# Performance work log

Hardware: AMD Instinct MI355X
Metric: run time of the kernel (lower is better)

The kernel has to match this reference:

```python
import jax, jax.numpy as jnp
import numpy as np

N = 50000      # nodes
E = 1600000    # directed edges (avg degree 32)
IN_DIM = 64
OUT_DIM = 64


def setup_inputs() -> dict:
    key = jax.random.key(0)
    ks = jax.random.split(key, 8)
    mu = jax.random.normal(ks[0], (N, IN_DIM), dtype=jnp.float32)
    x = jax.random.normal(ks[1], (N, 1), dtype=jnp.float32)
    edge_index = jax.random.randint(ks[2], (2, E), 0, N, dtype=jnp.int64)
    edge_w = jax.random.uniform(ks[3], (E,), dtype=jnp.float32)
    # torch nn.Linear(in, out, bias=False) weight has shape [out, in]
    W1 = jax.random.normal(ks[4], (OUT_DIM, 1), dtype=jnp.float32) * (1.0 / 1.0)
    W2 = jax.random.normal(ks[5], (OUT_DIM, 1), dtype=jnp.float32) * (1.0 / 1.0)
    W3 = jax.random.normal(ks[6], (OUT_DIM, IN_DIM), dtype=jnp.float32) * (1.0 / np.sqrt(IN_DIM))
    W4 = jax.random.normal(ks[7], (OUT_DIM, 3 * OUT_DIM), dtype=jnp.float32) * (1.0 / np.sqrt(3 * OUT_DIM))
    return {"mu": mu, "x": x, "edge_index": edge_index, "edge_w": edge_w,
            "W1": W1, "W2": W2, "W3": W3, "W4": W4}


def reference(mu, x, edge_index, edge_w, W1, W2, W3, W4):
    relu = jax.nn.relu
    n_nodes = mu.shape[0]
    # per-node / per-edge embeddings
    h_x = relu(x @ W1.T)                       # [N, out]
    h_e = relu(edge_w[:, None] @ W2.T)         # [E, out]
    h_mu = relu(mu @ W3.T)                     # [N, out]
    dst = edge_index[1]                        # gather side (reverse-direction message passing)
    src = edge_index[0]                        # scatter side
    # gather, concat along feature dim -> [E, 3*out]
    cat_feat = jnp.concatenate([h_x[dst], h_e, h_mu[dst]], axis=1)
    # scatter_add over destination row 0 -> [N, 3*out]
    agg = jax.ops.segment_sum(cat_feat, src, num_segments=n_nodes)
    agg = relu(agg @ W4.T)                     # [N, out]
    return relu(h_x + h_mu + agg)
```

## Files before the change

### kernel.cpp

```cpp
#include <hip/hip_runtime.h>


#define KBINS 512
#define BCHUNK 4096
#define CAPB 4096
#define CAPL 3500
#define MAXW 98

typedef __attribute__((ext_vector_type(8))) short short8;
typedef __attribute__((ext_vector_type(4))) float f32x4;
typedef __attribute__((ext_vector_type(4))) unsigned short u16x4;

__device__ inline unsigned short to_bf16(float f) {
    unsigned u = __float_as_uint(f);
    return (unsigned short)((u + 0x7FFFu + ((u >> 16) & 1u)) >> 16);
}

__global__ void k_prep(const float* __restrict__ W1, const float* __restrict__ W2,
                       const float* __restrict__ W3, const float* __restrict__ W4,
                       short* __restrict__ gB1, short* __restrict__ gB2,
                       float* __restrict__ gvec, unsigned* __restrict__ gcursor) {
    __shared__ float sa[64], sb[64];
    int t = threadIdx.x;
    gcursor[t] = 0u;
    gcursor[256 + t] = 0u;
    if (t < 64) {
        float w1 = W1[t];
        sa[t] = fmaxf(w1, 0.f);
        sb[t] = fmaxf(-w1, 0.f);
        gvec[t] = sa[t];
        gvec[64 + t] = sb[t];
    }
    __syncthreads();
    if (t < 64) {
        float s1 = 0.f, s2 = 0.f, s3 = 0.f;
#pragma unroll 8
        for (int o = 0; o < 64; ++o) {
            float w4a = W4[t * 192 + o];
            float w4b = W4[t * 192 + 64 + o];
            s1 += w4a * sa[o];
            s2 += w4a * sb[o];
            s3 += w4b * fmaxf(W2[o], 0.f);
        }
        gvec[128 + t] = s1;
        gvec[192 + t] = s2;
        gvec[256 + t] = s3;
    }
    for (int idx = t; idx < 4096; idx += 256) {
        int j = idx >> 6, k = idx & 63;
        int lane = ((k >> 3) & 3) * 16 + (j & 15);
        int pos = (((j >> 4) * 2 + (k >> 5)) * 64 + lane) * 8 + (k & 7);
        gB1[pos] = (short)to_bf16(W3[idx]);
        gB2[pos] = (short)to_bf16(W4[j * 192 + 128 + k]);
    }
}

__global__ void __launch_bounds__(512, 8) k_hb(
    const float* __restrict__ mu, const float* __restrict__ x,
    const short* __restrict__ gB1, const short* __restrict__ gB2,
    const float* __restrict__ gvec,
    unsigned short* __restrict__ base, unsigned short* __restrict__ hc2,
    const int* __restrict__ ei, const float* __restrict__ ew,
    unsigned* __restrict__ gcursor, unsigned* __restrict__ bins,
    int N, int E) {
    __shared__ __align__(16) char smem[35840];
    short* sB1 = (short*)smem;
    short* sB2 = (short*)(smem + 8192);
    float* sAv = (float*)(smem + 16384);
    float* sBv = (float*)(smem + 16640);
    float* sVA = (float*)(smem + 16896);
    float* sVB = (float*)(smem + 17152);
    short* sA  = (short*)(smem + 17408);
    unsigned* cnt   = (unsigned*)smem;
    unsigned* basel = (unsigned*)(smem + 2048);
    unsigned* gbase = (unsigned*)(smem + 4096);
    unsigned* wsum  = (unsigned*)(smem + 6144);
    unsigned* wpre  = (unsigned*)(smem + 6176);
    unsigned* stage = (unsigned*)(smem + 6208);
    unsigned short* binof = (unsigned short*)(smem + 22592);

    int t = threadIdx.x;
    int wave = t >> 6, l = t & 63;

    for (int i = t; i < 512; i += 512) {
        ((short8*)sB1)[i] = ((const short8*)gB1)[i];
        ((short8*)sB2)[i] = ((const short8*)gB2)[i];
    }
    if (t >= 512 - 256) {
        int v = t - (512 - 256);
        if (v < 64) sAv[v] = gvec[v];
        else if (v < 128) sBv[v - 64] = gvec[64 + (v - 64)];
        else if (v < 192) sVA[v - 128] = gvec[128 + (v - 128)];
        else sVB[v - 192] = gvec[192 + (v - 192)];
    }
    __syncthreads();

    int n0 = (blockIdx.x * 8 + wave) * 16;
    if (n0 < N) {
        short* A1 = sA + wave * 2304 / 2;
        {
            int srow = l >> 2, scol = (l & 3) * 16;
            bool rok = (n0 + srow) < N;
            const float4* gp = (const float4*)(mu + (size_t)(n0 + srow) * 64 + scol);
            float4 m0 = {}, m1 = {}, m2 = {}, m3 = {};
            if (rok) { m0 = gp[0]; m1 = gp[1]; m2 = gp[2]; m3 = gp[3]; }
            short8 v0, v1;
            v0[0]=to_bf16(m0.x); v0[1]=to_bf16(m0.y); v0[2]=to_bf16(m0.z); v0[3]=to_bf16(m0.w);
            v0[4]=to_bf16(m1.x); v0[5]=to_bf16(m1.y); v0[6]=to_bf16(m1.z); v0[7]=to_bf16(m1.w);
            v1[0]=to_bf16(m2.x); v1[1]=to_bf16(m2.y); v1[2]=to_bf16(m2.z); v1[3]=to_bf16(m2.w);
            v1[4]=to_bf16(m3.x); v1[5]=to_bf16(m3.y); v1[6]=to_bf16(m3.z); v1[7]=to_bf16(m3.w);
            *(short8*)&A1[srow * 72 + scol] = v0;
            *(short8*)&A1[srow * 72 + scol + 8] = v1;
        }
        float pr[4], qr[4];
#pragma unroll
        for (int r = 0; r < 4; ++r) {
            int nr = n0 + (l >> 4) * 4 + r;
            float xv = (nr < N) ? x[nr] : 0.f;
            pr[r] = fmaxf(xv, 0.f);
            qr[r] = fmaxf(-xv, 0.f);
        }
        f32x4 acc[4] = {};
        {
            short8 a0 = *(const short8*)&A1[(l & 15) * 72 + ((l >> 4) * 8)];
            short8 a1 = *(const short8*)&A1[(l & 15) * 72 + 32 + ((l >> 4) * 8)];
#pragma unroll
            for (int jt = 0; jt < 4; ++jt) {
                short8 b0 = *(const short8*)&sB1[((jt * 2 + 0) * 64 + l) * 8];
                short8 b1 = *(const short8*)&sB1[((jt * 2 + 1) * 64 + l) * 8];
                acc[jt] = __builtin_amdgcn_mfma_f32_16x16x32_bf16(a0, b0, acc[jt], 0, 0, 0);
                acc[jt] = __builtin_amdgcn_mfma_f32_16x16x32_bf16(a1, b1, acc[jt], 0, 0, 0);
            }
        }
#pragma unroll
        for (int jt = 0; jt < 4; ++jt) {
            int jc = jt * 16 + (l & 15);
            float aj = sAv[jc], bj = sBv[jc];
#pragma unroll
            for (int r = 0; r < 4; ++r) {
                int row = (l >> 4) * 4 + r;
                float h = fmaxf(acc[jt][r], 0.f);
                A1[row * 72 + jc] = (short)to_bf16(h);
                int nr = n0 + row;
                if (nr < N) base[(size_t)nr * 64 + jc] = to_bf16(pr[r] * aj + qr[r] * bj + h);
            }
        }
        f32x4 acc2[4] = {};
        {
            short8 a0 = *(const short8*)&A1[(l & 15) * 72 + ((l >> 4) * 8)];
            short8 a1 = *(const short8*)&A1[(l & 15) * 72 + 32 + ((l >> 4) * 8)];
#pragma unroll
            for (int jt = 0; jt < 4; ++jt) {
                short8 b0 = *(const short8*)&sB2[((jt * 2 + 0) * 64 + l) * 8];
                short8 b1 = *(const short8*)&sB2[((jt * 2 + 1) * 64 + l) * 8];
                acc2[jt] = __builtin_amdgcn_mfma_f32_16x16x32_bf16(a0, b0, acc2[jt], 0, 0, 0);
                acc2[jt] = __builtin_amdgcn_mfma_f32_16x16x32_bf16(a1, b1, acc2[jt], 0, 0, 0);
            }
        }
#pragma unroll
        for (int jt = 0; jt < 4; ++jt) {
            int jc = jt * 16 + (l & 15);
            float vaj = sVA[jc], vbj = sVB[jc];
#pragma unroll
            for (int r = 0; r < 4; ++r) {
                int nr = n0 + (l >> 4) * 4 + r;
                if (nr < N)
                    hc2[(size_t)nr * 64 + jc] =
                        to_bf16(acc2[jt][r] + pr[r] * vaj + qr[r] * vbj);
            }
        }
    }
    __syncthreads();

    for (int c0 = blockIdx.x * BCHUNK; c0 < E; c0 += gridDim.x * BCHUNK) {
        cnt[t] = 0;
        __syncthreads();
        int mybin[8]; unsigned myrank[8]; unsigned myrec[8]; bool ok[8];
#pragma unroll
        for (int k = 0; k < 8; ++k) {
            int e = c0 + t + k * 512;
            ok[k] = (e < E);
            if (ok[k]) {
                int s = ei[e];
                int d = ei[E + e];
                unsigned wq = (unsigned)(ew[e] * 512.0f + 0.5f);
                if (wq > 511u) wq = 511u;
                unsigned b = ((unsigned)s * (unsigned)KBINS) / (unsigned)N;
                unsigned start = ((unsigned)b * (unsigned)N + KBINS - 1) / KBINS;
                unsigned sl = (unsigned)s - start;
                myrec[k] = (unsigned)d | (sl << 16) | (wq << 23);
                mybin[k] = (int)b;
                myrank[k] = atomicAdd(&cnt[b], 1u);
            }
        }
        __syncthreads();
        {
            unsigned v = cnt[t];
            unsigned sc = v;
#pragma unroll
            for (int off = 1; off < 64; off <<= 1) {
                unsigned u = (unsigned)__shfl_up((int)sc, off, 64);
                if (l >= off) sc += u;
            }
            if (l == 63) wsum[wave] = sc;
            __syncthreads();
            if (t < 8) {
                unsigned s = 0;
                for (int i = 0; i < t; ++i) s += wsum[i];
                wpre[t] = s;
            }
            __syncthreads();
            unsigned excl = sc - v + wpre[wave];
            basel[t] = excl;
            if (v) gbase[t] = atomicAdd(&gcursor[t], v);
        }
        __syncthreads();
#pragma unroll
        for (int k = 0; k < 8; ++k) if (ok[k]) {
            unsigned pos = basel[mybin[k]] + myrank[k];
            stage[pos] = myrec[k];
            binof[pos] = (unsigned short)mybin[k];
        }
        __syncthreads();
        int total = E - c0; if (total > BCHUNK) total = BCHUNK;
#pragma unroll
        for (int k = 0; k < 8; ++k) {
            int i = t + k * 512;
            if (i < total) {
                int b = binof[i];
                unsigned dst = gbase[b] + (unsigned)i - basel[b];
                if (dst < CAPB) bins[(size_t)b * CAPB + dst] = stage[i];
            }
        }
        __syncthreads();
    }
}

__global__ void __launch_bounds__(1024) k_agg(
    const unsigned short* __restrict__ hc2, const unsigned short* __restrict__ base,
    const unsigned* __restrict__ gcursor, const unsigned* __restrict__ bins,
    const float* __restrict__ gvec, float* __restrict__ out, int N) {
    __shared__ unsigned srec[CAPL];
    __shared__ unsigned hist[128];
    __shared__ unsigned sbase[128];
    __shared__ __align__(16) float svs[64];
    int b = blockIdx.x;
    int t = threadIdx.x;
    if (t < 128) hist[t] = 0;
    if (t >= 128 && t < 192) svs[t - 128] = gvec[256 + (t - 128)];
    int start = (b * N + KBINS - 1) / KBINS;
    int endn  = ((b + 1) * N + KBINS - 1) / KBINS;
    if (endn > N) endn = N;
    int W = endn - start;
    if (W > MAXW) W = MAXW;
    __syncthreads();
    int cntb = (int)gcursor[b];
    if (cntb > CAPB) cntb = CAPB;
    const unsigned* rec = bins + (size_t)b * CAPB;
    unsigned r[4]; unsigned rank[4]; bool ok[4];
#pragma unroll
    for (int k = 0; k < 4; ++k) {
        int i = t + k * 1024;
        ok[k] = (i < cntb);
        if (ok[k]) {
            r[k] = rec[i];
            rank[k] = atomicAdd(&hist[(r[k] >> 16) & 0x7Fu], 1u);
        }
    }
    __syncthreads();
    if (t < 64) {
        unsigned h0 = hist[2 * t], h1 = hist[2 * t + 1];
        unsigned s = h0 + h1;
#pragma unroll
        for (int off = 1; off < 64; off <<= 1) {
            unsigned u = (unsigned)__shfl_up((int)s, off, 64);
            if (t >= off) s += u;
        }
        sbase[2 * t]     = s - h1 - h0;
        sbase[2 * t + 1] = s - h1;
    }
    __syncthreads();
#pragma unroll
    for (int k = 0; k < 4; ++k) if (ok[k]) {
        unsigned pos = sbase[(r[k] >> 16) & 0x7Fu] + rank[k];
        if (pos < CAPL) srec[pos] = r[k];
    }
    __syncthreads();
    int wave = t >> 6, l = t & 63;
    int g = l >> 4, m = l & 15;
    f32x4 vsv = *(const f32x4*)&svs[m * 4];
    const float sc512 = 1.0f / 512.0f;
    for (int sl = wave; sl < W; sl += 16) {
        int beg = (int)sbase[sl];
        int end = beg + (int)hist[sl];
        if (beg > CAPL) beg = CAPL;
        if (end > CAPL) end = CAPL;
        f32x4 acc = {0.f, 0.f, 0.f, 0.f};
        float swn = 0.f;
        int i = beg;
        for (; i + 8 <= end; i += 8) {
            unsigned r0 = srec[i + g];
            unsigned r1 = srec[i + 4 + g];
            u16x4 u0 = *(const u16x4*)(hc2 + (size_t)(r0 & 0xFFFFu) * 64 + m * 4);
            u16x4 u1 = *(const u16x4*)(hc2 + (size_t)(r1 & 0xFFFFu) * 64 + m * 4);
            acc[0] += __uint_as_float((unsigned)u0[0] << 16);
            acc[1] += __uint_as_float((unsigned)u0[1] << 16);
            acc[2] += __uint_as_float((unsigned)u0[2] << 16);
            acc[3] += __uint_as_float((unsigned)u0[3] << 16);
            acc[0] += __uint_as_float((unsigned)u1[0] << 16);
            acc[1] += __uint_as_float((unsigned)u1[1] << 16);
            acc[2] += __uint_as_float((unsigned)u1[2] << 16);
            acc[3] += __uint_as_float((unsigned)u1[3] << 16);
            swn += (float)(r0 >> 23) + (float)(r1 >> 23);
        }
        for (; i < end; i += 4) {
            if (i + g < end) {
                unsigned r0 = srec[i + g];
                u16x4 u0 = *(const u16x4*)(hc2 + (size_t)(r0 & 0xFFFFu) * 64 + m * 4);
                acc[0] += __uint_as_float((unsigned)u0[0] << 16);
                acc[1] += __uint_as_float((unsigned)u0[1] << 16);
                acc[2] += __uint_as_float((unsigned)u0[2] << 16);
                acc[3] += __uint_as_float((unsigned)u0[3] << 16);
                swn += (float)(r0 >> 23);
            }
        }
#pragma unroll
        for (int off = 16; off < 64; off <<= 1) {
            acc[0] += __shfl_xor(acc[0], off, 64);
            acc[1] += __shfl_xor(acc[1], off, 64);
            acc[2] += __shfl_xor(acc[2], off, 64);
            acc[3] += __shfl_xor(acc[3], off, 64);
            swn    += __shfl_xor(swn, off, 64);
        }
        if (g == 0) {
            size_t gi = (size_t)(start + sl) * 64 + m * 4;
            u16x4 bv = *(const u16x4*)(base + gi);
            f32x4 o;
#pragma unroll
            for (int k = 0; k < 4; ++k) {
                float aggv = fmaxf(swn * (vsv[k] * sc512) + acc[k], 0.f);
                float bval = __uint_as_float(((unsigned)bv[k]) << 16);
                o[k] = fmaxf(bval + aggv, 0.f);
            }
            *(f32x4*)&out[gi] = o;
        }
    }
}

extern "C" void kernel_launch(void* const* d_in, const int* in_sizes, int n_in,
                              void* d_out, int out_size, void* d_ws, size_t ws_size,
                              hipStream_t stream) {
    const float* mu = (const float*)d_in[0];
    const float* x  = (const float*)d_in[1];
    const int*   ei = (const int*)d_in[2];
    const float* ew = (const float*)d_in[3];
    const float* W1 = (const float*)d_in[4];
    const float* W2 = (const float*)d_in[5];
    const float* W3 = (const float*)d_in[6];
    const float* W4 = (const float*)d_in[7];
    float* out = (float*)d_out;

    const int N = in_sizes[1];
    const int E = in_sizes[3];

    unsigned short* base = (unsigned short*)d_ws;
    unsigned short* hc2 = base + (size_t)N * 64;
    unsigned* bins = (unsigned*)(hc2 + (size_t)N * 64);
    unsigned* gcursor = bins + (size_t)KBINS * CAPB;
    short* gB1 = (short*)(gcursor + KBINS);
    short* gB2 = gB1 + 4096;
    float* gvec = (float*)(gB2 + 4096);

    k_prep<<<1, 256, 0, stream>>>(W1, W2, W3, W4, gB1, gB2, gvec, gcursor);

    int hblocks = (N + 127) / 128;
    int chunks = (E + BCHUNK - 1) / BCHUNK;
    int grid = hblocks > chunks ? hblocks : chunks;
    k_hb<<<grid, 512, 0, stream>>>(mu, x, gB1, gB2, gvec, base, hc2,
                                   ei, ew, gcursor, bins, N, E);

    k_agg<<<KBINS, 1024, 0, stream>>>(hc2, base, gcursor, bins, gvec, out, N);
}
```

Measured before the change: 59.76 us.

## Split bf16 node table into two 32-column planes for narrower gathers

The per-node bf16 feature table hc2 is now stored as two planes of 32 columns each instead of one 64-column row. The aggregation kernel makes two passes, one per plane, and each lane gathers 16 bytes (8 bf16) with 16 edges in flight per wave rather than 4. The goal is a smaller per-pass gather working set that fits cache better, plus more memory-level parallelism per load instruction. In exchange, the edge records and segment bounds are read twice, the wave reduction now spans more shuffle steps, and the loop body holds more accumulators.

```diff
diff --git a/kernel.cpp b/kernel.cpp
--- a/kernel.cpp
+++ b/kernel.cpp
@@ -81,6 +81,7 @@
 
     int t = threadIdx.x;
     int wave = t >> 6, l = t & 63;
+    size_t PN = (size_t)N * 32;
 
     for (int i = t; i < 512; i += 512) {
         ((short8*)sB1)[i] = ((const short8*)gB1)[i];
@@ -161,11 +162,13 @@
         for (int jt = 0; jt < 4; ++jt) {
             int jc = jt * 16 + (l & 15);
             float vaj = sVA[jc], vbj = sVB[jc];
+            size_t pb = (size_t)(jt >> 1) * PN;
+            int col = (jt & 1) * 16 + (l & 15);
 #pragma unroll
             for (int r = 0; r < 4; ++r) {
                 int nr = n0 + (l >> 4) * 4 + r;
                 if (nr < N)
-                    hc2[(size_t)nr * 64 + jc] =
+                    hc2[pb + (size_t)nr * 32 + col] =
                         to_bf16(acc2[jt][r] + pr[r] * vaj + qr[r] * vbj);
             }
         }
@@ -287,62 +290,66 @@
     }
     __syncthreads();
     int wave = t >> 6, l = t & 63;
-    int g = l >> 4, m = l & 15;
-    f32x4 vsv = *(const f32x4*)&svs[m * 4];
+    int g = l >> 2, m = l & 3;
+    size_t PN = (size_t)N * 32;
     const float sc512 = 1.0f / 512.0f;
-    for (int sl = wave; sl < W; sl += 16) {
-        int beg = (int)sbase[sl];
-        int end = beg + (int)hist[sl];
-        if (beg > CAPL) beg = CAPL;
-        if (end > CAPL) end = CAPL;
-        f32x4 acc = {0.f, 0.f, 0.f, 0.f};
-        float swn = 0.f;
-        int i = beg;
-        for (; i + 8 <= end; i += 8) {
-            unsigned r0 = srec[i + g];
-            unsigned r1 = srec[i + 4 + g];
-            u16x4 u0 = *(const u16x4*)(hc2 + (size_t)(r0 & 0xFFFFu) * 64 + m * 4);
-            u16x4 u1 = *(const u16x4*)(hc2 + (size_t)(r1 & 0xFFFFu) * 64 + m * 4);
-            acc[0] += __uint_as_float((unsigned)u0[0] << 16);
-            acc[1] += __uint_as_float((unsigned)u0[1] << 16);
-            acc[2] += __uint_as_float((unsigned)u0[2] << 16);
-            acc[3] += __uint_as_float((unsigned)u0[3] << 16);
-            acc[0] += __uint_as_float((unsigned)u1[0] << 16);
-            acc[1] += __uint_as_float((unsigned)u1[1] << 16);
-            acc[2] += __uint_as_float((unsigned)u1[2] << 16);
-            acc[3] += __uint_as_float((unsigned)u1[3] << 16);
-            swn += (float)(r0 >> 23) + (float)(r1 >> 23);
-        }
-        for (; i < end; i += 4) {
-            if (i + g < end) {
+#pragma unroll
+    for (int p = 0; p < 2; ++p) {
+        const unsigned short* hp = hc2 + (size_t)p * PN;
+        int fb = p * 32 + m * 8;
+        f32x4 vs0 = *(const f32x4*)&svs[fb];
+        f32x4 vs1 = *(const f32x4*)&svs[fb + 4];
+        for (int sl = wave; sl < W; sl += 16) {
+            int beg = (int)sbase[sl];
+            int end = beg + (int)hist[sl];
+            if (beg > CAPL) beg = CAPL;
+            if (end > CAPL) end = CAPL;
+            float acc[8] = {0.f, 0.f, 0.f, 0.f, 0.f, 0.f, 0.f, 0.f};
+            float swn = 0.f;
+            int i = beg;
+            for (; i + 32 <= end; i += 32) {
                 unsigned r0 = srec[i + g];
-                u16x4 u0 = *(const u16x4*)(hc2 + (size_t)(r0 & 0xFFFFu) * 64 + m * 4);
-                acc[0] += __uint_as_float((unsigned)u0[0] << 16);
-                acc[1] += __uint_as_float((unsigned)u0[1] << 16);
-                acc[2] += __uint_as_float((unsigned)u0[2] << 16);
-                acc[3] += __uint_as_float((unsigned)u0[3] << 16);
-                swn += (float)(r0 >> 23);
-            }
-        }
-#pragma unroll
-        for (int off = 16; off < 64; off <<= 1) {
-            acc[0] += __shfl_xor(acc[0], off, 64);
-            acc[1] += __shfl_xor(acc[1], off, 64);
-            acc[2] += __shfl_xor(acc[2], off, 64);
-            acc[3] += __shfl_xor(acc[3], off, 64);
-            swn    += __shfl_xor(swn, off, 64);
-        }
-        if (g == 0) {
-            size_t gi = (size_t)(start + sl) * 64 + m * 4;
-            u16x4 bv = *(const u16x4*)(base + gi);
-            f32x4 o;
-#pragma unroll
-            for (int k = 0; k < 4; ++k) {
-                float aggv = fmaxf(swn * (vsv[k] * sc512) + acc[k], 0.f);
-                float bval = __uint_as_float(((unsigned)bv[k]) << 16);
-                o[k] = fmaxf(bval + aggv, 0.f);
-            }
-            *(f32x4*)&out[gi] = o;
+                unsigned r1 = srec[i + 16 + g];
+                short8 u0 = *(const short8*)(hp + (size_t)(r0 & 0xFFFFu) * 32 + m * 8);
+                short8 u1 = *(const short8*)(hp + (size_t)(r1 & 0xFFFFu) * 32 + m * 8);
+#pragma unroll
+                for (int k = 0; k < 8; ++k) {
+                    acc[k] += __uint_as_float(((unsigned)(unsigned short)u0[k]) << 16);
+                    acc[k] += __uint_as_float(((unsigned)(unsigned short)u1[k]) << 16);
+                }
+                swn += (float)(r0 >> 23) + (float)(r1 >> 23);
+            }
+            for (; i < end; i += 16) {
+                if (i + g < end) {
+                    unsigned r0 = srec[i + g];
+                    short8 u0 = *(const short8*)(hp + (size_t)(r0 & 0xFFFFu) * 32 + m * 8);
+#pragma unroll
+                    for (int k = 0; k < 8; ++k)
+                        acc[k] += __uint_as_float(((unsigned)(unsigned short)u0[k]) << 16);
+                    swn += (float)(r0 >> 23);
+                }
+            }
+#pragma unroll
+            for (int off = 4; off < 64; off <<= 1) {
+#pragma unroll
+                for (int k = 0; k < 8; ++k) acc[k] += __shfl_xor(acc[k], off, 64);
+                swn += __shfl_xor(swn, off, 64);
+            }
+            if (g == 0) {
+                size_t gi = (size_t)(start + sl) * 64 + fb;
+                u16x4 b0 = *(const u16x4*)(base + gi);
+                u16x4 b1 = *(const u16x4*)(base + gi + 4);
+                f32x4 o0, o1;
+#pragma unroll
+                for (int k = 0; k < 4; ++k) {
+                    float a0 = fmaxf(swn * (vs0[k] * sc512) + acc[k], 0.f);
+                    float a1 = fmaxf(swn * (vs1[k] * sc512) + acc[4 + k], 0.f);
+                    o0[k] = fmaxf(__uint_as_float(((unsigned)b0[k]) << 16) + a0, 0.f);
+                    o1[k] = fmaxf(__uint_as_float(((unsigned)b1[k]) << 16) + a1, 0.f);
+                }
+                *(f32x4*)&out[gi] = o0;
+                *(f32x4*)&out[gi + 4] = o1;
+            }
         }
     }
 }
```

Result: slower. 83.92 us (+40.4%).
